# Kernel tuning notes

Hardware: AMD Instinct MI355X
Metric: run time of the kernel (lower is better)

## Reference

```python
import jax, jax.numpy as jnp
import numpy as np

B, V, H, L = 256, 50000, 1024, 2

def setup_inputs() -> dict:
    key = jax.random.key(0)
    ks = jax.random.split(key, 9)
    s = 1.0 / np.sqrt(H)
    return {
        "input_ids": jax.random.randint(ks[0], (B,), 0, V),
        "hidden": jax.random.normal(ks[1], (L, B, H), jnp.float32),
        "emb": jax.random.normal(ks[2], (V, H), jnp.float32) * 0.02,
        "w_ih": jax.random.uniform(ks[3], (L, 3 * H, H), jnp.float32, -s, s),
        "w_hh": jax.random.uniform(ks[4], (L, 3 * H, H), jnp.float32, -s, s),
        "b_ih": jax.random.uniform(ks[5], (L, 3 * H), jnp.float32, -s, s),
        "b_hh": jax.random.uniform(ks[6], (L, 3 * H), jnp.float32, -s, s),
        "dec_w": jax.random.uniform(ks[7], (V, H), jnp.float32, -s, s),
        "dec_b": jax.random.uniform(ks[8], (V,), jnp.float32, -s, s),
    }

def _gru_cell(x, h, w_ih_l, w_hh_l, b_ih_l, b_hh_l):
    # PyTorch GRU cell math. x: [B,H], h: [B,H]
    gi = x @ w_ih_l.T + b_ih_l          # [B, 3H]
    gh = h @ w_hh_l.T + b_hh_l          # [B, 3H]
    i_r, i_z, i_n = jnp.split(gi, 3, axis=-1)
    h_r, h_z, h_n = jnp.split(gh, 3, axis=-1)
    r = jax.nn.sigmoid(i_r + h_r)
    z = jax.nn.sigmoid(i_z + h_z)
    n = jnp.tanh(i_n + r * h_n)
    return (1.0 - z) * n + z * h

def reference(input_ids, hidden, emb, w_ih, w_hh, b_ih, b_hh, dec_w, dec_b):
    x = emb[input_ids]                  # embedding gather: [B, H]
    new_h = []
    for l in range(hidden.shape[0]):    # small fixed n_layers loop
        h_new = _gru_cell(x, hidden[l], w_ih[l], w_hh[l], b_ih[l], b_hh[l])
        new_h.append(h_new)
        x = h_new                       # output of layer l feeds layer l+1
    hidden_out = jnp.stack(new_h)       # [L, B, H]
    logits = x @ dec_w.T + dec_b        # [B, V]
    return logits, hidden_out
```

## Files before the change

kernel.cpp:

```cpp
#include <hip/hip_runtime.h>

#define KDIM 1024

typedef __attribute__((ext_vector_type(8))) short bf16x8;
typedef __attribute__((ext_vector_type(4))) short short4v;
typedef __attribute__((ext_vector_type(4))) float f32x4;

__device__ __forceinline__ short f2bf(float f) {
    union { float f; unsigned u; } x; x.f = f;
    unsigned r = x.u + 0x7fffu + ((x.u >> 16) & 1u);
    return (short)(r >> 16);
}

__device__ __forceinline__ bf16x8 cvt8(f32x4 a, f32x4 b) {
    union { unsigned u[4]; bf16x8 v; } r;
    asm("v_cvt_pk_bf16_f32 %0, %1, %2" : "=v"(r.u[0]) : "v"(a.x), "v"(a.y));
    asm("v_cvt_pk_bf16_f32 %0, %1, %2" : "=v"(r.u[1]) : "v"(a.z), "v"(a.w));
    asm("v_cvt_pk_bf16_f32 %0, %1, %2" : "=v"(r.u[2]) : "v"(b.x), "v"(b.y));
    asm("v_cvt_pk_bf16_f32 %0, %1, %2" : "=v"(r.u[3]) : "v"(b.z), "v"(b.w));
    return r.v;
}

__device__ __forceinline__ void gload16(const void* g, void* l) {
    __builtin_amdgcn_global_load_lds(
        (const __attribute__((address_space(1))) void*)g,
        (__attribute__((address_space(3))) void*)l, 16, 0, 0);
}

#define WAIT_VM(n) asm volatile("s_waitcnt vmcnt(" #n ")" ::: "memory")
#define BARRIER() do { asm volatile("" ::: "memory"); \
                       __builtin_amdgcn_s_barrier();  \
                       asm volatile("" ::: "memory"); } while (0)

template<int NF, bool PRED>
__launch_bounds__(256, 2)
__global__ void gemm_pipe(const short* __restrict__ A0, const float* __restrict__ W0,
                          float* __restrict__ C0, int nb0,
                          const short* __restrict__ A1, const float* __restrict__ W1,
                          float* __restrict__ C1,
                          const float* __restrict__ bias, int N, int ldc)
{
    constexpr int WBYTES = NF * 4096;
    constexpr int BUFB   = 16384 + WBYTES;
    __shared__ __align__(1024) char lds[3 * BUFB];

    const int bx = blockIdx.x;
    const short* A; const float* W; float* C; int n0;
    if (bx < nb0) { A = A0; W = W0; C = C0; n0 = bx * (32 * NF); }
    else          { A = A1; W = W1; C = C1; n0 = (bx - nb0) * (32 * NF); }

    const int t = threadIdx.x;
    const int lane = t & 63;
    const int w = t >> 6;
    const int wr = w >> 1;
    const int wc = w & 1;

    const float* gW[NF];
    #pragma unroll
    for (int i = 0; i < NF; ++i) {
        int sl = (i * 4 + w) * 64 + lane;
        int row = sl >> 3, cc = sl & 7;
        int rowg = n0 + row;
        if (PRED) rowg = (rowg < N) ? rowg : (N - 1);
        gW[i] = W + (size_t)rowg * KDIM + ((cc ^ (row & 7)) << 2);
    }
    const short* gA[4];
    #pragma unroll
    for (int j = 0; j < 4; ++j)
        gA[j] = A + (size_t)(j * 4 + w) * 16384 + lane * 8;

    f32x4 acc[8][NF];
    #pragma unroll
    for (int i = 0; i < 8; ++i)
        #pragma unroll
        for (int j = 0; j < NF; ++j)
            acc[i][j] = (f32x4){0.f, 0.f, 0.f, 0.f};

    auto stage = [&](int s, int buf) {
        char* base = lds + buf * BUFB;
        #pragma unroll
        for (int i = 0; i < NF; ++i)
            gload16(gW[i] + s * 32, base + 16384 + (i * 4 + w) * 1024);
        #pragma unroll
        for (int j = 0; j < 4; ++j)
            gload16(gA[j] + s * 512, base + (j * 4 + w) * 1024);
    };

    auto compute = [&](int buf) {
        const char* base = lds + buf * BUFB;
        const char* Wb = base + 16384;
        bf16x8 bfr[NF];
        #pragma unroll
        for (int nf = 0; nf < NF; ++nf) {
            int row = (wc * NF + nf) * 16 + (lane & 15);
            int c0 = (lane >> 4) << 1;
            f32x4 lo = *(const f32x4*)(Wb + row * 128 + ((c0 ^ (row & 7)) << 4));
            f32x4 hi = *(const f32x4*)(Wb + row * 128 + (((c0 + 1) ^ (row & 7)) << 4));
            bfr[nf] = cvt8(lo, hi);
        }
        #pragma unroll
        for (int mf = 0; mf < 8; ++mf) {
            bf16x8 a = *(const bf16x8*)(base + (wr * 8 + mf) * 1024 + lane * 16);
            #pragma unroll
            for (int nf = 0; nf < NF; ++nf)
                acc[mf][nf] = __builtin_amdgcn_mfma_f32_16x16x32_bf16(a, bfr[nf], acc[mf][nf], 0, 0, 0);
        }
    };

    stage(0, 0);
    stage(1, 1);

    int bc = 0, bp = 2;
    for (int s = 0; s < 32; ++s) {
        if (s + 2 < 32) {
            stage(s + 2, bp);
            if constexpr (NF == 2) WAIT_VM(12); else WAIT_VM(10);
        } else if (s + 2 == 32) {
            if constexpr (NF == 2) WAIT_VM(6); else WAIT_VM(5);
        } else {
            WAIT_VM(0);
        }
        BARRIER();
        compute(bc);
        BARRIER();
        bc = (bc == 2) ? 0 : bc + 1;
        bp = (bp == 2) ? 0 : bp + 1;
    }

    #pragma unroll
    for (int mf = 0; mf < 8; ++mf) {
        int row = wr * 128 + mf * 16 + ((lane >> 4) << 2);
        #pragma unroll
        for (int nf = 0; nf < NF; ++nf) {
            int col = n0 + (wc * NF + nf) * 16 + (lane & 15);
            if (PRED && col >= N) continue;
            float bv = bias ? bias[col] : 0.0f;
            #pragma unroll
            for (int r = 0; r < 4; ++r)
                C[(size_t)(row + r) * ldc + col] = acc[mf][nf][r] + bv;
        }
    }
}

__global__ void prep_kernel(const int* __restrict__ ids, const float* __restrict__ hidden,
                            const float* __restrict__ emb,
                            short* __restrict__ x_frag, short* __restrict__ h_frag)
{
    const int m = blockIdx.x;
    const int which = blockIdx.y;
    const int j = threadIdx.x << 3;

    const float* src;
    short* dst;
    if (which == 0) { src = emb + (size_t)ids[m] * KDIM; dst = x_frag; }
    else {
        src = hidden + ((size_t)(which - 1) * 256 + m) * KDIM;
        dst = h_frag + (size_t)(which - 1) * 256 * KDIM;
    }
    f32x4 v0 = *(const f32x4*)(src + j);
    f32x4 v1 = *(const f32x4*)(src + j + 4);
    int mf = m >> 4, rr = m & 15, kf = j >> 5, g = (j >> 3) & 3;
    short* p = dst + (size_t)((mf * 32 + kf) * 64 + g * 16 + rr) * 8;
    short4v a, b;
    a.x = f2bf(v0.x); a.y = f2bf(v0.y); a.z = f2bf(v0.z); a.w = f2bf(v0.w);
    b.x = f2bf(v1.x); b.y = f2bf(v1.y); b.z = f2bf(v1.z); b.w = f2bf(v1.w);
    *(short4v*)p = a;
    *(short4v*)(p + 4) = b;
}

__global__ void gate_kernel(const float* __restrict__ gi, const float* __restrict__ gh,
                            const float* __restrict__ bi, const float* __restrict__ bh,
                            const float* __restrict__ hprev, float* __restrict__ hout,
                            short* __restrict__ x_frag)
{
    const int m = blockIdx.x;
    const int j = threadIdx.x << 3;
    const float* gim = gi + (size_t)m * 3072;
    const float* ghm = gh + (size_t)m * 3072;
    const float* hp = hprev + (size_t)m * KDIM;
    float* ho = hout + (size_t)m * KDIM;
    int mf = m >> 4, rr = m & 15, kf = j >> 5, g = (j >> 3) & 3;
    short* xp = x_frag + (size_t)((mf * 32 + kf) * 64 + g * 16 + rr) * 8;

    #pragma unroll
    for (int half = 0; half < 2; ++half) {
        int jj = j + half * 4;
        f32x4 vir = *(const f32x4*)(gim + jj);
        f32x4 viz = *(const f32x4*)(gim + 1024 + jj);
        f32x4 vin = *(const f32x4*)(gim + 2048 + jj);
        f32x4 vhr = *(const f32x4*)(ghm + jj);
        f32x4 vhz = *(const f32x4*)(ghm + 1024 + jj);
        f32x4 vhn = *(const f32x4*)(ghm + 2048 + jj);
        f32x4 bir = *(const f32x4*)(bi + jj);
        f32x4 biz = *(const f32x4*)(bi + 1024 + jj);
        f32x4 bin = *(const f32x4*)(bi + 2048 + jj);
        f32x4 bhr = *(const f32x4*)(bh + jj);
        f32x4 bhz = *(const f32x4*)(bh + 1024 + jj);
        f32x4 bhn = *(const f32x4*)(bh + 2048 + jj);
        f32x4 vh  = *(const f32x4*)(hp + jj);
        f32x4 outv;
        short4v xb;
        #pragma unroll
        for (int e = 0; e < 4; ++e) {
            float r = 1.f / (1.f + __expf(-(vir[e] + bir[e] + vhr[e] + bhr[e])));
            float z = 1.f / (1.f + __expf(-(viz[e] + biz[e] + vhz[e] + bhz[e])));
            float n = tanhf(vin[e] + bin[e] + r * (vhn[e] + bhn[e]));
            outv[e] = (1.f - z) * n + z * vh[e];
        }
        *(f32x4*)(ho + jj) = outv;
        xb.x = f2bf(outv[0]); xb.y = f2bf(outv[1]); xb.z = f2bf(outv[2]); xb.w = f2bf(outv[3]);
        *(short4v*)(xp + half * 4) = xb;
    }
}

extern "C" void kernel_launch(void* const* d_in, const int* in_sizes, int n_in,
                              void* d_out, int out_size, void* d_ws, size_t ws_size,
                              hipStream_t stream)
{
    const int*   ids    = (const int*)d_in[0];
    const float* hidden = (const float*)d_in[1];
    const float* emb    = (const float*)d_in[2];
    const float* w_ih   = (const float*)d_in[3];
    const float* w_hh   = (const float*)d_in[4];
    const float* b_ih   = (const float*)d_in[5];
    const float* b_hh   = (const float*)d_in[6];
    const float* dec_w  = (const float*)d_in[7];
    const float* dec_b  = (const float*)d_in[8];

    float* out = (float*)d_out;
    float* logits = out;
    float* hidden_out = out + (size_t)256 * 50000;

    short* x_frag = (short*)d_ws;
    short* h_frag = x_frag + 256 * 1024;
    float* gi = logits;
    float* gh = logits + (size_t)256 * 3072;

    prep_kernel<<<dim3(256, 3), 128, 0, stream>>>(ids, hidden, emb, x_frag, h_frag);

    for (int l = 0; l < 2; ++l) {
        gemm_pipe<1, false><<<192, 256, 0, stream>>>(
            x_frag, w_ih + (size_t)l * 3072 * 1024, gi, 96,
            h_frag + (size_t)l * 256 * 1024, w_hh + (size_t)l * 3072 * 1024, gh,
            nullptr, 3072, 3072);
        gate_kernel<<<256, 128, 0, stream>>>(
            gi, gh, b_ih + (size_t)l * 3072, b_hh + (size_t)l * 3072,
            hidden + (size_t)l * 256 * 1024,
            hidden_out + (size_t)l * 256 * 1024, x_frag);
    }

    gemm_pipe<2, true><<<782, 256, 0, stream>>>(
        x_frag, dec_w, logits, 782,
        x_frag, dec_w, logits,
        dec_b, 50000, 50000);
}
```

Before: 128.7 us.

## Add dedicated large-tile decoder GEMM kernel with 256-column blocks

Replaces the generic 64-column-per-block decoder GEMM (782 blocks of 256 threads) with a new kernel of 512 threads per block, each block covering 256 output columns and all 256 batch rows, for 196 blocks total. Each wave computes an 8x4 grid of 16x16 MFMA tiles, with a three-stage LDS pipeline that loads fp32 weights and bf16 activations through global_load_lds. The larger tile means each activation block is loaded far fewer times and the grid maps onto the CUs in about one wave. In exchange it uses much more LDS (about 144KB) and more registers, allowing only one block per CU, which lowers occupancy and the ability to hide latency.

After: 124.8 us. -3.0%, faster.

```diff
diff --git a/kernel.cpp b/kernel.cpp
--- a/kernel.cpp
+++ b/kernel.cpp
@@ -31,6 +31,111 @@
 #define BARRIER() do { asm volatile("" ::: "memory"); \
                        __builtin_amdgcn_s_barrier();  \
                        asm volatile("" ::: "memory"); } while (0)
+
+__launch_bounds__(512, 1)
+__global__ void gemm_dec(const short* __restrict__ A, const float* __restrict__ W,
+                         float* __restrict__ C, const float* __restrict__ bias, int N)
+{
+    constexpr int BUFB = 49152;
+    __shared__ __align__(1024) char lds[3 * BUFB];
+
+    const int n0 = blockIdx.x * 256;
+    const int t = threadIdx.x;
+    const int lane = t & 63;
+    const int w = t >> 6;
+    const int wr = w >> 2;
+    const int wc = w & 3;
+
+    const short* gA[2];
+    #pragma unroll
+    for (int i = 0; i < 2; ++i)
+        gA[i] = A + (size_t)(w * 2 + i) * 16384 + lane * 8;
+    const float* gW[4];
+    int wdst[4];
+    #pragma unroll
+    for (int i = 0; i < 4; ++i) {
+        int q = w * 4 + i;
+        int kc = q >> 3, hf = (q >> 2) & 1, j = q & 3;
+        int colg = n0 + j * 64 + lane;
+        colg = (colg < N) ? colg : (N - 1);
+        gW[i] = W + (size_t)colg * KDIM + kc * 8 + hf * 4;
+        wdst[i] = 16384 + kc * 8192 + hf * 4096 + j * 1024;
+    }
+
+    f32x4 acc[8][4];
+    #pragma unroll
+    for (int i = 0; i < 8; ++i)
+        #pragma unroll
+        for (int j = 0; j < 4; ++j)
+            acc[i][j] = (f32x4){0.f, 0.f, 0.f, 0.f};
+
+    auto stage = [&](int s, int buf) {
+        char* base = lds + buf * BUFB;
+        #pragma unroll
+        for (int i = 0; i < 4; ++i)
+            gload16(gW[i] + s * 32, base + wdst[i]);
+        #pragma unroll
+        for (int i = 0; i < 2; ++i)
+            gload16(gA[i] + s * 512, base + (w * 2 + i) * 1024);
+    };
+
+    const int kc = lane >> 4;
+    const int cl = lane & 15;
+
+    auto compute = [&](int buf) {
+        const char* base = lds + buf * BUFB;
+        const char* Wb = base + 16384;
+        bf16x8 bfr[4];
+        #pragma unroll
+        for (int nf = 0; nf < 4; ++nf) {
+            const char* p = Wb + kc * 8192 + (wc * 64 + nf * 16 + cl) * 16;
+            f32x4 lo = *(const f32x4*)(p);
+            f32x4 hi = *(const f32x4*)(p + 4096);
+            bfr[nf] = cvt8(lo, hi);
+        }
+        #pragma unroll
+        for (int mf = 0; mf < 8; ++mf) {
+            bf16x8 a = *(const bf16x8*)(base + (wr * 8 + mf) * 1024 + lane * 16);
+            #pragma unroll
+            for (int nf = 0; nf < 4; ++nf)
+                acc[mf][nf] = __builtin_amdgcn_mfma_f32_16x16x32_bf16(a, bfr[nf], acc[mf][nf], 0, 0, 0);
+        }
+    };
+
+    stage(0, 0);
+    stage(1, 1);
+
+    int bc = 0, bp = 2;
+    for (int s = 0; s < 32; ++s) {
+        if (s + 2 < 32) {
+            stage(s + 2, bp);
+            WAIT_VM(12);
+        } else if (s + 2 == 32) {
+            WAIT_VM(6);
+        } else {
+            WAIT_VM(0);
+        }
+        BARRIER();
+        compute(bc);
+        BARRIER();
+        bc = (bc == 2) ? 0 : bc + 1;
+        bp = (bp == 2) ? 0 : bp + 1;
+    }
+
+    #pragma unroll
+    for (int mf = 0; mf < 8; ++mf) {
+        int row = wr * 128 + mf * 16 + ((lane >> 4) << 2);
+        #pragma unroll
+        for (int nf = 0; nf < 4; ++nf) {
+            int col = n0 + wc * 64 + nf * 16 + cl;
+            if (col >= N) continue;
+            float bv = bias[col];
+            #pragma unroll
+            for (int r = 0; r < 4; ++r)
+                C[(size_t)(row + r) * N + col] = acc[mf][nf][r] + bv;
+        }
+    }
+}
 
 template<int NF, bool PRED>
 __launch_bounds__(256, 2)
@@ -249,8 +354,5 @@
             hidden_out + (size_t)l * 256 * 1024, x_frag);
     }
 
-    gemm_pipe<2, true><<<782, 256, 0, stream>>>(
-        x_frag, dec_w, logits, 782,
-        x_frag, dec_w, logits,
-        dec_b, 50000, 50000);
-}
+    gemm_dec<<<196, 512, 0, stream>>>(x_frag, dec_w, logits, dec_b, 50000);
+}
```

## Replace decoder GEMM with persistent 512-thread kernel streaming 256-column weight tiles

Applied to the files above, without the earlier changes.

Adds a dedicated decoder GEMM kernel in which each of 196 blocks owns 256 output columns and walks them in 8 groups of 32. Weight rows are loaded into registers, converted to bf16 and stored to a swizzled, double-buffered LDS slot while the previous group is being computed. A-fragments are read straight from global memory (so they hit in cache), and the full batch of 256 rows is covered by 8 waves. The intent is to cut the block count to about one per CU and overlap the fp32 weight stream with MFMA work. The cost is a single block per CU with a heavy register-staging footprint, and per-group output writes that may limit latency hiding.

Result: slower. 360.2 us (+179.9%).

```diff
diff --git a/kernel.cpp b/kernel.cpp
--- a/kernel.cpp
+++ b/kernel.cpp
@@ -5,6 +5,7 @@
 typedef __attribute__((ext_vector_type(8))) short bf16x8;
 typedef __attribute__((ext_vector_type(4))) short short4v;
 typedef __attribute__((ext_vector_type(4))) float f32x4;
+typedef __attribute__((ext_vector_type(2))) unsigned uint2v;
 
 __device__ __forceinline__ short f2bf(float f) {
     union { float f; unsigned u; } x; x.f = f;
@@ -27,10 +28,114 @@
         (__attribute__((address_space(3))) void*)l, 16, 0, 0);
 }
 
-#define WAIT_VM(n) asm volatile("s_waitcnt vmcnt(" #n ")" ::: "memory")
+#define WAIT_VM(n)  asm volatile("s_waitcnt vmcnt(" #n ")" ::: "memory")
+#define WAIT_LGKM() asm volatile("s_waitcnt lgkmcnt(0)" ::: "memory")
 #define BARRIER() do { asm volatile("" ::: "memory"); \
                        __builtin_amdgcn_s_barrier();  \
                        asm volatile("" ::: "memory"); } while (0)
+
+__launch_bounds__(512, 1)
+__global__ void gemm_dec2(const short* __restrict__ A, const float* __restrict__ W,
+                          float* __restrict__ C, const float* __restrict__ bias, int N)
+{
+    __shared__ __align__(1024) char lds[2][65536];
+
+    const int n0 = blockIdx.x * 256;
+    const int t = threadIdx.x;
+    const int lane = t & 63;
+    const int w = t >> 6;
+    const int cl = lane & 15;
+    const int kc = lane >> 4;
+
+    f32x4 stg[16];
+
+    auto issue = [&](int g) {
+        #pragma unroll
+        for (int j = 0; j < 16; ++j) {
+            const int u = w * 16 + j, rr = u >> 2, q = u & 3;
+            int row = n0 + g * 32 + rr;
+            row = (row < N) ? row : (N - 1);
+            stg[j] = *(const f32x4*)(W + (size_t)row * KDIM + q * 256 + lane * 4);
+        }
+    };
+
+    auto store_lds = [&](int slot) {
+        char* base = lds[slot];
+        #pragma unroll
+        for (int j = 0; j < 16; ++j) {
+            const int u = w * 16 + j, rr = u >> 2, q = u & 3;
+            unsigned lo, hi;
+            asm("v_cvt_pk_bf16_f32 %0, %1, %2" : "=v"(lo) : "v"(stg[j].x), "v"(stg[j].y));
+            asm("v_cvt_pk_bf16_f32 %0, %1, %2" : "=v"(hi) : "v"(stg[j].z), "v"(stg[j].w));
+            int c = q * 32 + (lane >> 1);
+            int addr = rr * 2048 + ((c ^ (rr & 7)) << 4) + ((lane & 1) << 3);
+            uint2v d; d.x = lo; d.y = hi;
+            *(uint2v*)(base + addr) = d;
+        }
+    };
+
+    f32x4 acc[2][2];
+
+    auto compute = [&](int slot) {
+        const char* base = lds[slot];
+        const int sw = (cl & 7);
+        const int rb0 = cl * 2048;
+        #pragma unroll
+        for (int kf = 0; kf < 32; ++kf) {
+            bf16x8 a0 = *(const bf16x8*)(A + (size_t)(((w * 2 + 0) * 32 + kf) * 64 + lane) * 8);
+            bf16x8 a1 = *(const bf16x8*)(A + (size_t)(((w * 2 + 1) * 32 + kf) * 64 + lane) * 8);
+            int boff = rb0 + (((kf * 4 + kc) ^ sw) << 4);
+            bf16x8 b0 = *(const bf16x8*)(base + boff);
+            bf16x8 b1 = *(const bf16x8*)(base + boff + 32768);
+            acc[0][0] = __builtin_amdgcn_mfma_f32_16x16x32_bf16(a0, b0, acc[0][0], 0, 0, 0);
+            acc[0][1] = __builtin_amdgcn_mfma_f32_16x16x32_bf16(a0, b1, acc[0][1], 0, 0, 0);
+            acc[1][0] = __builtin_amdgcn_mfma_f32_16x16x32_bf16(a1, b0, acc[1][0], 0, 0, 0);
+            acc[1][1] = __builtin_amdgcn_mfma_f32_16x16x32_bf16(a1, b1, acc[1][1], 0, 0, 0);
+        }
+    };
+
+    auto cwrite = [&](int g) {
+        #pragma unroll
+        for (int m = 0; m < 2; ++m) {
+            int row = (w * 2 + m) * 16 + kc * 4;
+            #pragma unroll
+            for (int nf = 0; nf < 2; ++nf) {
+                int col = n0 + g * 32 + nf * 16 + cl;
+                if (col < N) {
+                    float bv = bias[col];
+                    #pragma unroll
+                    for (int r = 0; r < 4; ++r)
+                        C[(size_t)(row + r) * N + col] = acc[m][nf][r] + bv;
+                }
+            }
+        }
+    };
+
+    issue(0);
+    WAIT_VM(0);
+    store_lds(0);
+    issue(1);
+    WAIT_LGKM();
+    BARRIER();
+
+    for (int g = 0; g < 8; ++g) {
+        #pragma unroll
+        for (int i = 0; i < 2; ++i)
+            #pragma unroll
+            for (int j = 0; j < 2; ++j)
+                acc[i][j] = (f32x4){0.f, 0.f, 0.f, 0.f};
+
+        compute(g & 1);
+        if (g + 1 < 8) {
+            WAIT_VM(0);
+            store_lds((g + 1) & 1);
+            if (g + 2 < 8) issue(g + 2);
+            WAIT_LGKM();
+            BARRIER();
+        }
+        cwrite(g);
+    }
+}
 
 template<int NF, bool PRED>
 __launch_bounds__(256, 2)
@@ -249,8 +354,5 @@
             hidden_out + (size_t)l * 256 * 1024, x_frag);
     }
 
-    gemm_pipe<2, true><<<782, 256, 0, stream>>>(
-        x_frag, dec_w, logits, 782,
-        x_frag, dec_w, logits,
-        dec_b, 50000, 50000);
-}
+    gemm_dec2<<<196, 512, 0, stream>>>(x_frag, dec_w, logits, dec_b, 50000);
+}
```

## Add dedicated decoder GEMM kernel with A read from global and streamed W

Applied to the files above, without the earlier changes.

Replaces the generic pipelined GEMM for the 256x50000 decoder projection with a new kernel. Each 512-thread block owns 128 output columns and works through them in four 32-column groups. Only the fp32 weight rows are staged in LDS, double-buffered and XOR-swizzled, while the bf16 activation fragments are read straight from global memory or cache. The goal is to stream dec_w once using fewer, larger blocks with higher occupancy. The trade-off is repeated global reads of the small A matrix in exchange for less LDS traffic and a different launch geometry.

After: 126.1 us. -2.1%, faster.

```diff
diff --git a/kernel.cpp b/kernel.cpp
--- a/kernel.cpp
+++ b/kernel.cpp
@@ -27,10 +27,113 @@
         (__attribute__((address_space(3))) void*)l, 16, 0, 0);
 }
 
-#define WAIT_VM(n) asm volatile("s_waitcnt vmcnt(" #n ")" ::: "memory")
+#define WAIT_VM(n)  asm volatile("s_waitcnt vmcnt(" #n ")" ::: "memory")
 #define BARRIER() do { asm volatile("" ::: "memory"); \
                        __builtin_amdgcn_s_barrier();  \
                        asm volatile("" ::: "memory"); } while (0)
+
+__launch_bounds__(512, 4)
+__global__ void gemm_dec3(const short* __restrict__ A, const float* __restrict__ W,
+                          float* __restrict__ C, const float* __restrict__ bias, int N)
+{
+    __shared__ __align__(1024) char lds[2][32768];
+
+    const int n0 = blockIdx.x * 128;
+    const int t = threadIdx.x;
+    const int lane = t & 63;
+    const int w = t >> 6;
+    const int cl = lane & 15;
+    const int kc = lane >> 4;
+
+    int perm[4];
+    #pragma unroll
+    for (int i = 0; i < 4; ++i) {
+        int rr = w * 4 + i;
+        perm[i] = (lane & ~7) | ((lane & 7) ^ (rr & 7));
+    }
+
+    float bv[4][2];
+    #pragma unroll
+    for (int rg = 0; rg < 4; ++rg)
+        #pragma unroll
+        for (int nf = 0; nf < 2; ++nf) {
+            int col = n0 + rg * 32 + nf * 16 + cl;
+            bv[rg][nf] = bias[col < N ? col : 0];
+        }
+
+    auto stage = [&](int g) {
+        const int rg = g >> 2, kq = g & 3;
+        char* base = lds[g & 1];
+        #pragma unroll
+        for (int i = 0; i < 4; ++i) {
+            int rr = w * 4 + i;
+            int rowg = n0 + rg * 32 + rr;
+            rowg = (rowg < N) ? rowg : (N - 1);
+            gload16(W + (size_t)rowg * KDIM + kq * 256 + perm[i] * 4,
+                    base + rr * 1024);
+        }
+    };
+
+    f32x4 acc[2][2];
+
+    auto compute = [&](int g) {
+        const int kq = g & 3;
+        const char* r0 = lds[g & 1] + cl * 1024;
+        const int s = cl & 7;
+        #pragma unroll
+        for (int kf = 0; kf < 8; ++kf) {
+            const int kfg = kq * 8 + kf;
+            bf16x8 a0 = *(const bf16x8*)(A + (size_t)((w * 2 + 0) * 32 + kfg) * 512 + lane * 8);
+            bf16x8 a1 = *(const bf16x8*)(A + (size_t)((w * 2 + 1) * 32 + kfg) * 512 + lane * 8);
+            const int qlo = kf * 8 + ((kc * 2) ^ s);
+            const int qhi = kf * 8 + ((kc * 2 + 1) ^ s);
+            f32x4 lo0 = *(const f32x4*)(r0 + qlo * 16);
+            f32x4 hi0 = *(const f32x4*)(r0 + qhi * 16);
+            f32x4 lo1 = *(const f32x4*)(r0 + 16384 + qlo * 16);
+            f32x4 hi1 = *(const f32x4*)(r0 + 16384 + qhi * 16);
+            bf16x8 b0 = cvt8(lo0, hi0);
+            bf16x8 b1 = cvt8(lo1, hi1);
+            acc[0][0] = __builtin_amdgcn_mfma_f32_16x16x32_bf16(a0, b0, acc[0][0], 0, 0, 0);
+            acc[0][1] = __builtin_amdgcn_mfma_f32_16x16x32_bf16(a0, b1, acc[0][1], 0, 0, 0);
+            acc[1][0] = __builtin_amdgcn_mfma_f32_16x16x32_bf16(a1, b0, acc[1][0], 0, 0, 0);
+            acc[1][1] = __builtin_amdgcn_mfma_f32_16x16x32_bf16(a1, b1, acc[1][1], 0, 0, 0);
+        }
+    };
+
+    stage(0);
+    stage(1);
+
+    for (int g = 0; g < 16; ++g) {
+        WAIT_VM(4);
+        BARRIER();
+        if ((g & 3) == 0) {
+            #pragma unroll
+            for (int i = 0; i < 2; ++i)
+                #pragma unroll
+                for (int j = 0; j < 2; ++j)
+                    acc[i][j] = (f32x4){0.f, 0.f, 0.f, 0.f};
+        }
+        compute(g);
+        BARRIER();
+        if (g + 2 < 16) stage(g + 2);
+        if ((g & 3) == 3) {
+            const int rg = g >> 2;
+            #pragma unroll
+            for (int m = 0; m < 2; ++m) {
+                int row = (w * 2 + m) * 16 + kc * 4;
+                #pragma unroll
+                for (int nf = 0; nf < 2; ++nf) {
+                    int col = n0 + rg * 32 + nf * 16 + cl;
+                    if (col < N) {
+                        #pragma unroll
+                        for (int r = 0; r < 4; ++r)
+                            C[(size_t)(row + r) * N + col] = acc[m][nf][r] + bv[rg][nf];
+                    }
+                }
+            }
+        }
+    }
+}
 
 template<int NF, bool PRED>
 __launch_bounds__(256, 2)
@@ -134,10 +237,10 @@
         for (int nf = 0; nf < NF; ++nf) {
             int col = n0 + (wc * NF + nf) * 16 + (lane & 15);
             if (PRED && col >= N) continue;
-            float bv = bias ? bias[col] : 0.0f;
+            float bvv = bias ? bias[col] : 0.0f;
             #pragma unroll
             for (int r = 0; r < 4; ++r)
-                C[(size_t)(row + r) * ldc + col] = acc[mf][nf][r] + bv;
+                C[(size_t)(row + r) * ldc + col] = acc[mf][nf][r] + bvv;
         }
     }
 }
@@ -249,8 +352,5 @@
             hidden_out + (size_t)l * 256 * 1024, x_frag);
     }
 
-    gemm_pipe<2, true><<<782, 256, 0, stream>>>(
-        x_frag, dec_w, logits, 782,
-        x_frag, dec_w, logits,
-        dec_b, 50000, 50000);
-}
+    gemm_dec3<<<392, 512, 0, stream>>>(x_frag, dec_w, logits, dec_b, 50000);
+}
```
